# Kernel tuning notes

Hardware: AMD Instinct MI355X
Metric: run time of the kernel (lower is better)

The kernel has to match this reference:

```python
import jax, jax.numpy as jnp
import numpy as np

FP8_E4M3_MAX = 448.0  # matches the 448.0 constant in the torch module


def setup_inputs() -> dict:
    key = jax.random.key(0)
    kx, kw, kb = jax.random.split(key, 3)
    B, S, D_IN, D_OUT = 4, 2048, 4096, 4096
    x = jax.random.normal(kx, (B, S, D_IN), dtype=jnp.float32)
    # Simulate the __init__-time FP8 quantization of the linear weight.
    w = jax.random.normal(kw, (D_OUT, D_IN), dtype=jnp.float32) * 0.02
    amax = jnp.max(jnp.abs(w))
    weight_scale = FP8_E4M3_MAX / (amax + 1e-12)
    weight_fp8 = (w * weight_scale).astype(jnp.float8_e4m3fn)  # stored FP8 buffer
    weight_inv_scale = (1.0 / weight_scale).astype(jnp.float32)
    bias = jax.random.normal(kb, (D_OUT,), dtype=jnp.float32) * 0.02
    return {"x": x, "weight_fp8": weight_fp8,
            "weight_inv_scale": weight_inv_scale, "bias": bias}


def reference(x, weight_fp8, weight_inv_scale, bias):
    # forward: dequantize FP8 weight to compute dtype, scale, then dense linear
    w = weight_fp8.astype(x.dtype) * weight_inv_scale.astype(x.dtype)  # [D_OUT, D_IN]
    # F.linear(x, w, bias) == x @ w.T + bias
    return jnp.einsum('bsd,od->bso', x, w) + bias.astype(x.dtype)
```

## Files before the change

### kernel.cpp

```cpp
#include <hip/hip_runtime.h>
#include <hip/hip_bf16.h>
#include <stdint.h>
#include <stddef.h>

typedef __bf16 bf16x8 __attribute__((ext_vector_type(8)));
typedef float  f32x4  __attribute__((ext_vector_type(4)));

__device__ __forceinline__ float fp8e4m3_to_f32(uint32_t b) {
    uint32_t e = (b >> 3) & 15u, m = b & 7u;
    float mag;
    if (e == 0)
        mag = (float)m * (1.0f / 512.0f);
    else
        mag = __uint_as_float(((e + 120u) << 23) | (m << 20));
    return (b & 0x80u) ? -mag : mag;
}

__device__ __forceinline__ unsigned short f32_to_bf16_bits(float f) {
    uint32_t x = __float_as_uint(f);
    uint32_t r = x + 0x7fffu + ((x >> 16) & 1u);
    return (unsigned short)(r >> 16);
}

__device__ __forceinline__ void gload_lds16(const void* g, void* l) {
    __builtin_amdgcn_global_load_lds(
        (const __attribute__((address_space(1))) uint32_t*)g,
        (__attribute__((address_space(3))) uint32_t*)l,
        16, 0, 0);
}

__global__ void detect_kernel(const uint32_t* __restrict__ w,
                              uint32_t* __restrict__ flag) {
    __shared__ int sF, sB;
    if (threadIdx.x == 0) { sF = 1; sB = 1; }
    __syncthreads();
    int f32ok = 1, bf16ok = 1;
    #pragma unroll
    for (int i = 0; i < 16; ++i) {
        uint32_t u = w[threadIdx.x * 16 + i];
        if (u & 0x000FFFFFu) f32ok = 0;
        if (u & 0x000F000Fu) bf16ok = 0;
    }
    if (!f32ok)  atomicExch(&sF, 0);
    if (!bf16ok) atomicExch(&sB, 0);
    __syncthreads();
    if (threadIdx.x == 0)
        *flag = sF ? 0u : (sB ? 1u : 2u);
}

__global__ void cvt_x_kernel(const float* __restrict__ x,
                             unsigned short* __restrict__ out, size_t n8) {
    size_t stride = (size_t)gridDim.x * blockDim.x;
    for (size_t i = (size_t)blockIdx.x * blockDim.x + threadIdx.x; i < n8; i += stride) {
        const float4* p = (const float4*)(x + i * 8);
        float4 a = p[0], b = p[1];
        union { uint4 v; unsigned short s[8]; } o;
        o.s[0] = f32_to_bf16_bits(a.x); o.s[1] = f32_to_bf16_bits(a.y);
        o.s[2] = f32_to_bf16_bits(a.z); o.s[3] = f32_to_bf16_bits(a.w);
        o.s[4] = f32_to_bf16_bits(b.x); o.s[5] = f32_to_bf16_bits(b.y);
        o.s[6] = f32_to_bf16_bits(b.z); o.s[7] = f32_to_bf16_bits(b.w);
        *(uint4*)(out + i * 8) = o.v;
    }
}

__global__ void prep_w_kernel(const void* __restrict__ wsrc,
                              const uint32_t* __restrict__ flag,
                              unsigned short* __restrict__ out, size_t n8) {
    const uint32_t mode = *flag;
    size_t stride = (size_t)gridDim.x * blockDim.x;
    for (size_t i = (size_t)blockIdx.x * blockDim.x + threadIdx.x; i < n8; i += stride) {
        union { uint4 v; unsigned short s[8]; } o;
        if (mode == 0) {
            const float4* p = (const float4*)((const float*)wsrc + i * 8);
            float4 a = p[0], b = p[1];
            o.s[0] = f32_to_bf16_bits(a.x); o.s[1] = f32_to_bf16_bits(a.y);
            o.s[2] = f32_to_bf16_bits(a.z); o.s[3] = f32_to_bf16_bits(a.w);
            o.s[4] = f32_to_bf16_bits(b.x); o.s[5] = f32_to_bf16_bits(b.y);
            o.s[6] = f32_to_bf16_bits(b.z); o.s[7] = f32_to_bf16_bits(b.w);
        } else if (mode == 1) {
            o.v = *(const uint4*)((const unsigned short*)wsrc + i * 8);
        } else {
            union { uint2 v; uint8_t b[8]; } u;
            u.v = *(const uint2*)((const uint8_t*)wsrc + i * 8);
            #pragma unroll
            for (int j = 0; j < 8; ++j)
                o.s[j] = f32_to_bf16_bits(fp8e4m3_to_f32(u.b[j]));
        }
        *(uint4*)(out + i * 8) = o.v;
    }
}


#define GBM 256
#define GBN 256
#define GBK 64

#define PH_IN() do {                                                           \
    __builtin_amdgcn_s_barrier();                                              \
    __builtin_amdgcn_s_setprio(1);                                             \
} while (0)

#define PH_OUT() do {                                                          \
    __builtin_amdgcn_s_setprio(0);                                             \
    __builtin_amdgcn_s_barrier();                                              \
} while (0)

#define LDA_(qm) do {                                                          \
    _Pragma("unroll") for (int m = 0; m < 4; ++m) {                            \
        Af[m][0] = *(const bf16x8*)(a0 + ((qm)*8192 + m*2048));                \
        Af[m][1] = *(const bf16x8*)(a1 + ((qm)*8192 + m*2048));                \
    }                                                                          \
} while (0)

#define LDB_(qn, Bf) do {                                                      \
    _Pragma("unroll") for (int n = 0; n < 2; ++n) {                            \
        Bf[n][0] = *(const bf16x8*)(b0 + ((qn)*4096 + n*2048));                \
        Bf[n][1] = *(const bf16x8*)(b1 + ((qn)*4096 + n*2048));                \
    }                                                                          \
} while (0)

#define MFMA_(qm, qn, Bf) do {                                                 \
    _Pragma("unroll") for (int m = 0; m < 4; ++m)                              \
    _Pragma("unroll") for (int n = 0; n < 2; ++n)                              \
    _Pragma("unroll") for (int ks = 0; ks < 2; ++ks)                           \
        acc[(qm)*4+m][(qn)*2+n] = __builtin_amdgcn_mfma_f32_16x16x32_bf16(     \
            Af[m][ks], Bf[n][ks], acc[(qm)*4+m][(qn)*2+n], 0, 0, 0);           \
} while (0)

#define STAGE_(gsrc, koff, ldst) do {                                          \
    const uint8_t* _p = (gsrc) + (koff);                                       \
    _Pragma("unroll") for (int j = 0; j < 4; ++j)                              \
        gload_lds16(_p + (size_t)j * 64 * KB2, (ldst) + (sdst + j*8192));      \
} while (0)

__global__ __launch_bounds__(512, 2)
void gemm256_8ph(const unsigned short* __restrict__ A,
                 const unsigned short* __restrict__ Bw,
                 const float* __restrict__ invp,
                 const float* __restrict__ bias,
                 float* __restrict__ C, int M, int N, int K) {
    __shared__ unsigned short lds[2][2][GBM * GBK];
    char* ldsb = (char*)&lds[0][0][0];

    const size_t KB2 = (size_t)K * 2;
    const int KT = K / GBK;

    const int nwg = gridDim.x;
    const int b   = blockIdx.x;
    const int wg  = (b & 7) * (nwg >> 3) + (b >> 3);
    const int MT  = M / GBM;
    const int tm  = wg % MT;
    const int tn  = wg / MT;

    const int t     = threadIdx.x;
    const int lane  = t & 63;
    const int wid   = t >> 6;
    const int wm    = wid >> 2;
    const int wn    = wid & 3;
    const int laneQ = lane & 15;
    const int laneH = lane >> 4;
    const int xorv  = (laneQ & 7) << 4;
    const int lrow  = lane >> 3;
    const int lcb   = (lane & 7) ^ lrow;

    const int col0  = (0   + laneH * 16) ^ xorv;
    const int col1  = (64  + laneH * 16) ^ xorv;
    const int aoff0 = wm * 16384 + laneQ * 128 + col0;
    const int aoff1 = wm * 16384 + laneQ * 128 + col1;
    const int boff0 = wn * 8192  + laneQ * 128 + col0;
    const int boff1 = wn * 8192  + laneQ * 128 + col1;
    const int sdst  = wid * 1024 + lane * 16;

    const uint8_t* gA = (const uint8_t*)A +
        ((size_t)tm * GBM + wid * 8 + lrow) * KB2 + (size_t)lcb * 16;
    const uint8_t* gB = (const uint8_t*)Bw +
        ((size_t)tn * GBN + wid * 8 + lrow) * KB2 + (size_t)lcb * 16;

    f32x4 acc[8][4] = {};
    bf16x8 Af[4][2], B0[2][2], B1[2][2];

    STAGE_(gB, (size_t)0,   ldsb + 32768);
    STAGE_(gA, (size_t)0,   ldsb);
    STAGE_(gB, (size_t)128, ldsb + 65536 + 32768);
    STAGE_(gA, (size_t)128, ldsb + 65536);
    asm volatile("s_waitcnt vmcnt(8)" ::: "memory");
    __builtin_amdgcn_s_barrier();

    for (int kt = 0; kt < KT; ++kt) {
        const int coff = (kt & 1) << 16;
        const char* ldsA = ldsb + coff;
        const char* ldsB = ldsb + coff + 32768;
        const char* a0 = ldsA + aoff0;
        const char* a1 = ldsA + aoff1;
        const char* b0 = ldsB + boff0;
        const char* b1 = ldsB + boff1;
        char* ldsAw = (char*)ldsA;
        char* ldsBw = (char*)ldsB;
        const bool more = (kt + 2) < KT;
        const size_t kb2 = (size_t)(kt + 2) * 128;

        LDA_(0);
        LDB_(0, B0);
        PH_IN();  MFMA_(0, 0, B0);  PH_OUT();

        LDB_(1, B1);
        PH_IN();  MFMA_(0, 1, B1);  PH_OUT();

        LDA_(1);
        if (more) STAGE_(gB, kb2, ldsBw);
        PH_IN();  MFMA_(1, 1, B1);  PH_OUT();

        if (more) STAGE_(gA, kb2, ldsAw);
        __builtin_amdgcn_s_setprio(1);
        MFMA_(1, 0, B0);
        __builtin_amdgcn_s_setprio(0);
        if (more) asm volatile("s_waitcnt vmcnt(8)" ::: "memory");
        else      asm volatile("s_waitcnt vmcnt(0)" ::: "memory");
        __builtin_amdgcn_s_barrier();
    }

    const float inv = *invp;
    float bv[4];
    #pragma unroll
    for (int n = 0; n < 4; ++n)
        bv[n] = bias[tn * GBN + wn * 64 + n * 16 + laneQ];

    #pragma unroll
    for (int m = 0; m < 8; ++m) {
        int rowb = tm * GBM + wm * 128 + m * 16 + laneH * 4;
        #pragma unroll
        for (int j = 0; j < 4; ++j) {
            float* cp = C + (size_t)(rowb + j) * N + tn * GBN + wn * 64;
            #pragma unroll
            for (int n = 0; n < 4; ++n)
                cp[n * 16 + laneQ] = acc[m][n][j] * inv + bv[n];
        }
    }
}

__global__ void naive_kernel(const float* __restrict__ x,
                             const void* __restrict__ wsrc,
                             const uint32_t* flag,
                             const float* __restrict__ invp,
                             const float* __restrict__ bias,
                             float* __restrict__ out, int M, int N, int K) {
    const uint32_t mode = flag ? *flag : 0u;
    size_t idx = (size_t)blockIdx.x * blockDim.x + threadIdx.x;
    if (idx >= (size_t)M * N) return;
    int m = (int)(idx / N), n = (int)(idx % N);
    const float* xr = x + (size_t)m * K;
    float s = 0.f;
    if (mode == 0) {
        const float* wr = (const float*)wsrc + (size_t)n * K;
        for (int k = 0; k < K; ++k) s += xr[k] * wr[k];
    } else if (mode == 1) {
        const unsigned short* wr = (const unsigned short*)wsrc + (size_t)n * K;
        for (int k = 0; k < K; ++k)
            s += xr[k] * __uint_as_float(((uint32_t)wr[k]) << 16);
    } else {
        const uint8_t* wr = (const uint8_t*)wsrc + (size_t)n * K;
        for (int k = 0; k < K; ++k) s += xr[k] * fp8e4m3_to_f32(wr[k]);
    }
    out[idx] = s * (*invp) + bias[n];
}

extern "C" void kernel_launch(void* const* d_in, const int* in_sizes, int n_in,
                              void* d_out, int out_size, void* d_ws, size_t ws_size,
                              hipStream_t stream) {
    const float*    x    = (const float*)d_in[0];
    const void*     wsrc = d_in[1];
    const float*    inv  = (const float*)d_in[2];
    const float*    bias = (const float*)d_in[3];
    float*          out  = (float*)d_out;

    const int K = in_sizes[1] / in_sizes[3];
    const int N = in_sizes[3];
    const int M = in_sizes[0] / K;

    const size_t needA = (size_t)M * K * sizeof(unsigned short);
    const size_t needB = (size_t)N * K * sizeof(unsigned short);

    const bool shape_ok = (M % GBM) == 0 && (N % GBN) == 0 && (K % GBK) == 0 &&
                          (K / GBK) >= 2 &&
                          (((M / GBM) * (N / GBN)) % 8) == 0;

    if (ws_size < needA + needB + 256 || !shape_ok) {
        size_t total = (size_t)M * N;
        uint32_t* flag = (ws_size >= 256) ? (uint32_t*)d_ws : nullptr;
        if (flag) detect_kernel<<<1, 256, 0, stream>>>((const uint32_t*)wsrc, flag);
        naive_kernel<<<(unsigned)((total + 255) / 256), 256, 0, stream>>>(
            x, wsrc, flag, inv, bias, out, M, N, K);
        return;
    }

    uint32_t*       flag = (uint32_t*)d_ws;
    unsigned short* Abf  = (unsigned short*)((char*)d_ws + 256);
    unsigned short* Wbf  = (unsigned short*)((char*)d_ws + 256 + needA);

    detect_kernel<<<1, 256, 0, stream>>>((const uint32_t*)wsrc, flag);
    cvt_x_kernel<<<2048, 256, 0, stream>>>(x, Abf, (size_t)M * K / 8);
    prep_w_kernel<<<2048, 256, 0, stream>>>(wsrc, flag, Wbf, (size_t)N * K / 8);

    dim3 grid((M / GBM) * (N / GBN));
    gemm256_8ph<<<grid, 512, 0, stream>>>(Abf, Wbf, inv, bias, out, M, N, K);
}
```

Measured before the change: 300.4 us.

## Switch bf16 GEMM from 16x16x32 to 32x32x16 MFMA tiles

```diff
diff --git a/kernel.cpp b/kernel.cpp
--- a/kernel.cpp
+++ b/kernel.cpp
@@ -4,7 +4,7 @@
 #include <stddef.h>
 
 typedef __bf16 bf16x8 __attribute__((ext_vector_type(8)));
-typedef float  f32x4  __attribute__((ext_vector_type(4)));
+typedef float  f32x16 __attribute__((ext_vector_type(16)));
 
 __device__ __forceinline__ float fp8e4m3_to_f32(uint32_t b) {
     uint32_t e = (b >> 3) & 15u, m = b & 7u;
@@ -106,25 +106,21 @@
 } while (0)
 
 #define LDA_(qm) do {                                                          \
-    _Pragma("unroll") for (int m = 0; m < 4; ++m) {                            \
-        Af[m][0] = *(const bf16x8*)(a0 + ((qm)*8192 + m*2048));                \
-        Af[m][1] = *(const bf16x8*)(a1 + ((qm)*8192 + m*2048));                \
-    }                                                                          \
-} while (0)
-
-#define LDB_(qn, Bf) do {                                                      \
-    _Pragma("unroll") for (int n = 0; n < 2; ++n) {                            \
-        Bf[n][0] = *(const bf16x8*)(b0 + ((qn)*4096 + n*2048));                \
-        Bf[n][1] = *(const bf16x8*)(b1 + ((qn)*4096 + n*2048));                \
-    }                                                                          \
-} while (0)
-
-#define MFMA_(qm, qn, Bf) do {                                                 \
-    _Pragma("unroll") for (int m = 0; m < 4; ++m)                              \
-    _Pragma("unroll") for (int n = 0; n < 2; ++n)                              \
-    _Pragma("unroll") for (int ks = 0; ks < 2; ++ks)                           \
-        acc[(qm)*4+m][(qn)*2+n] = __builtin_amdgcn_mfma_f32_16x16x32_bf16(     \
-            Af[m][ks], Bf[n][ks], acc[(qm)*4+m][(qn)*2+n], 0, 0, 0);           \
+    _Pragma("unroll") for (int mt = 0; mt < 2; ++mt)                           \
+    _Pragma("unroll") for (int ks = 0; ks < 4; ++ks)                           \
+        Af[mt][ks] = *(const bf16x8*)(ldsA + aoffK[ks] + ((qm)*2+mt)*4096);    \
+} while (0)
+
+#define LDB_(nt, Bf) do {                                                      \
+    _Pragma("unroll") for (int ks = 0; ks < 4; ++ks)                           \
+        Bf[ks] = *(const bf16x8*)(ldsB + boffK[ks] + (nt)*4096);               \
+} while (0)
+
+#define MFMA_(qm, nt, Bf) do {                                                 \
+    _Pragma("unroll") for (int ks = 0; ks < 4; ++ks)                           \
+    _Pragma("unroll") for (int mt = 0; mt < 2; ++mt)                           \
+        acc[(qm)*2+mt][nt] = __builtin_amdgcn_mfma_f32_32x32x16_bf16(          \
+            Af[mt][ks], Bf[ks], acc[(qm)*2+mt][nt], 0, 0, 0);                  \
 } while (0)
 
 #define STAGE_(gsrc, koff, ldst) do {                                          \
@@ -157,27 +153,28 @@
     const int wid   = t >> 6;
     const int wm    = wid >> 2;
     const int wn    = wid & 3;
-    const int laneQ = lane & 15;
-    const int laneH = lane >> 4;
-    const int xorv  = (laneQ & 7) << 4;
+    const int l31   = lane & 31;
+    const int h16   = (lane >> 5) * 16;
+    const int swz   = (lane & 7) << 4;
     const int lrow  = lane >> 3;
     const int lcb   = (lane & 7) ^ lrow;
 
-    const int col0  = (0   + laneH * 16) ^ xorv;
-    const int col1  = (64  + laneH * 16) ^ xorv;
-    const int aoff0 = wm * 16384 + laneQ * 128 + col0;
-    const int aoff1 = wm * 16384 + laneQ * 128 + col1;
-    const int boff0 = wn * 8192  + laneQ * 128 + col0;
-    const int boff1 = wn * 8192  + laneQ * 128 + col1;
-    const int sdst  = wid * 1024 + lane * 16;
+    int aoffK[4], boffK[4];
+    #pragma unroll
+    for (int ks = 0; ks < 4; ++ks) {
+        const int colb = (ks * 32 + h16) ^ swz;
+        aoffK[ks] = (wm * 128 + l31) * 128 + colb;
+        boffK[ks] = (wn * 64  + l31) * 128 + colb;
+    }
+    const int sdst = wid * 1024 + lane * 16;
 
     const uint8_t* gA = (const uint8_t*)A +
         ((size_t)tm * GBM + wid * 8 + lrow) * KB2 + (size_t)lcb * 16;
     const uint8_t* gB = (const uint8_t*)Bw +
         ((size_t)tn * GBN + wid * 8 + lrow) * KB2 + (size_t)lcb * 16;
 
-    f32x4 acc[8][4] = {};
-    bf16x8 Af[4][2], B0[2][2], B1[2][2];
+    f32x16 acc[4][2] = {};
+    bf16x8 Af[2][4], B0[4], B1[4];
 
     STAGE_(gB, (size_t)0,   ldsb + 32768);
     STAGE_(gA, (size_t)0,   ldsb);
@@ -190,10 +187,6 @@
         const int coff = (kt & 1) << 16;
         const char* ldsA = ldsb + coff;
         const char* ldsB = ldsb + coff + 32768;
-        const char* a0 = ldsA + aoff0;
-        const char* a1 = ldsA + aoff1;
-        const char* b0 = ldsB + boff0;
-        const char* b1 = ldsB + boff1;
         char* ldsAw = (char*)ldsA;
         char* ldsBw = (char*)ldsB;
         const bool more = (kt + 2) < KT;
@@ -220,20 +213,19 @@
     }
 
     const float inv = *invp;
-    float bv[4];
+    const int h5 = lane >> 5;
+    const float bv0 = bias[tn * GBN + wn * 64 + l31];
+    const float bv1 = bias[tn * GBN + wn * 64 + 32 + l31];
+
     #pragma unroll
-    for (int n = 0; n < 4; ++n)
-        bv[n] = bias[tn * GBN + wn * 64 + n * 16 + laneQ];
-
-    #pragma unroll
-    for (int m = 0; m < 8; ++m) {
-        int rowb = tm * GBM + wm * 128 + m * 16 + laneH * 4;
+    for (int mt = 0; mt < 4; ++mt) {
+        const int rowb = tm * GBM + wm * 128 + mt * 32 + h5 * 4;
         #pragma unroll
-        for (int j = 0; j < 4; ++j) {
-            float* cp = C + (size_t)(rowb + j) * N + tn * GBN + wn * 64;
-            #pragma unroll
-            for (int n = 0; n < 4; ++n)
-                cp[n * 16 + laneQ] = acc[m][n][j] * inv + bv[n];
+        for (int r = 0; r < 16; ++r) {
+            const int row = rowb + (r & 3) + 8 * (r >> 2);
+            float* cp = C + (size_t)row * N + tn * GBN + wn * 64 + l31;
+            cp[0]  = acc[mt][0][r] * inv + bv0;
+            cp[32] = acc[mt][1][r] * inv + bv1;
         }
     }
 }
```

Result: slower. 326.3 us (+8.6%).
